# Performance work log

Hardware: AMD Instinct MI355X
Metric: run time of the kernel (lower is better)

## Reference

```python
import jax, jax.numpy as jnp
import numpy as np

NUM_HEADS = 16
HEAD_DIM = 80  # embed_dim 1280 / 16


def setup_inputs() -> dict:
    key = jax.random.key(0)
    ks = jax.random.split(key, 5)
    E = NUM_HEADS * HEAD_DIM
    sq, b = 1024, 8
    x = jax.random.normal(ks[0], (sq, b, E), dtype=jnp.float32)
    w_in = jax.random.normal(ks[1], (E, 3 * E), dtype=jnp.float32) * (E ** -0.5)
    b_in = jax.random.normal(ks[2], (3 * E,), dtype=jnp.float32) * 0.01
    w_out = jax.random.normal(ks[3], (E, E), dtype=jnp.float32) * (E ** -0.5)
    b_out = jax.random.normal(ks[4], (E,), dtype=jnp.float32) * 0.01
    return {"x": x, "w_in": w_in, "b_in": b_in, "w_out": w_out, "b_out": b_out}


def reference(x, w_in, b_in, w_out, b_out):
    sq, b, E = x.shape
    H, D = NUM_HEADS, HEAD_DIM
    norm_factor = jnp.asarray(D ** 0.5, x.dtype)
    # in_proj: [sq, b, 3E] -> [sq, b, H, 3D], split into q/k/v along last dim
    mixed = (x @ w_in + b_in).reshape(sq, b, H, 3 * D)
    q, k, v = jnp.split(mixed, 3, axis=-1)  # each [sq, b, H, D]
    # merge (b, H) and move to batch-of-bmm layout [b*H, sq, D]
    q = q.reshape(sq, b * H, D).transpose(1, 0, 2) / norm_factor
    k = k.reshape(sq, b * H, D).transpose(1, 0, 2)
    v = v.reshape(sq, b * H, D).transpose(1, 0, 2)
    scores = jnp.einsum('nqd,nkd->nqk', q, k)  # [b*H, sq, sq]
    probs = jax.nn.softmax(scores, axis=-1)
    ctx = jnp.einsum('nqk,nkd->nqd', probs, v)  # [b*H, sq, D]
    # [b, H, sq, D] -> [sq, b, H, D] -> [sq, b, E]
    ctx = ctx.reshape(b, H, sq, D).transpose(2, 0, 1, 3).reshape(sq, b, E)
    return ctx @ w_out + b_out
```

## Files before the change

kernel.cpp:

```cpp
#include <hip/hip_runtime.h>

#define DEVI __device__ __forceinline__

typedef _Float16 f16x8 __attribute__((ext_vector_type(8)));
typedef _Float16 f16x4v __attribute__((ext_vector_type(4)));
typedef _Float16 f16x2 __attribute__((ext_vector_type(2)));
typedef __fp16 fp16x2 __attribute__((ext_vector_type(2)));
typedef float f32x4 __attribute__((ext_vector_type(4)));
typedef float f32x16 __attribute__((ext_vector_type(16)));
typedef unsigned u32x4 __attribute__((ext_vector_type(4)));

DEVI void gl16(const void* g, void* l) {
  __builtin_amdgcn_global_load_lds((const __attribute__((address_space(1))) void*)g,
                                   (__attribute__((address_space(3))) void*)l, 16, 0, 0);
}

#define VMCNT(N) asm volatile("s_waitcnt vmcnt(" #N ")" ::: "memory")
#define LGKM0() asm volatile("s_waitcnt lgkmcnt(0)" ::: "memory")
#define BARRIER() asm volatile("s_barrier" ::: "memory")

#if __has_builtin(__builtin_amdgcn_exp2f)
#define EXP2(x) __builtin_amdgcn_exp2f(x)
#else
#define EXP2(x) exp2f(x)
#endif

DEVI unsigned pk2(float a, float b) {
  fp16x2 t = __builtin_amdgcn_cvt_pkrtz(a, b);
  return __builtin_bit_cast(unsigned, t);
}
DEVI void pl32swap(unsigned &a, unsigned &b) {
  asm volatile("v_permlane32_swap_b32 %0, %1" : "+v"(a), "+v"(b));
}
DEVI float max3f(float a, float b, float c) {
  float d;
  asm("v_max3_f32 %0, %1, %2, %3" : "=v"(d) : "v"(a), "v"(b), "v"(c));
  return d;
}

__global__ __launch_bounds__(256) void k_prep(const float* __restrict__ x, _Float16* __restrict__ xb,
                                              const float* __restrict__ w_in, _Float16* __restrict__ w_inT,
                                              const float* __restrict__ w_out, _Float16* __restrict__ w_outT) {
  __shared__ float t[32][33];
  int bid = blockIdx.x;
  int tid = threadIdx.x;
  if (bid < 2048) {
    const int n4 = 8192 * 1280 / 4;
    for (int i = bid * 256 + tid; i < n4; i += 2048 * 256) {
      float4 v = ((const float4*)x)[i];
      f16x4v h = { (_Float16)v.x, (_Float16)v.y, (_Float16)v.z, (_Float16)v.w };
      ((f16x4v*)xb)[i] = h;
    }
    return;
  }
  const float* in; _Float16* out; int R, C, tIdx; bool perm;
  if (bid < 6848) { in = w_in;  out = w_inT;  R = 1280; C = 3840; tIdx = bid - 2048; perm = true; }
  else            { in = w_out; out = w_outT; R = 1280; C = 1280; tIdx = bid - 6848; perm = false; }
  int ntc = C / 32;
  int cb = (tIdx % ntc) * 32, rb = (tIdx / ntc) * 32;
  int tx = tid & 31, ty = tid >> 5;
  #pragma unroll
  for (int i = ty; i < 32; i += 8) t[i][tx] = in[(size_t)(rb + i) * C + cb + tx];
  __syncthreads();
  #pragma unroll
  for (int i = ty; i < 32; i += 8) {
    int c = cb + i;
    if (perm) {
      int hq = c / 240, tt = c - hq * 240;
      int reg = tt / 80, d = tt - reg * 80;
      c = reg * 1280 + hq * 80 + d;
    }
    out[(size_t)c * R + rb + tx] = (_Float16)t[tx][i];
  }
}


#define MM(NLO, AF, BF) do {                                                                       \
    __builtin_amdgcn_s_setprio(1);                                                                 \
    _Pragma("unroll")                                                                              \
    for (int m_ = 0; m_ < 8; m_++) {                                                               \
      acc[m_][NLO]     = __builtin_amdgcn_mfma_f32_16x16x32_f16(AF[m_], BF[NLO],     acc[m_][NLO],     0, 0, 0); \
      acc[m_][NLO + 1] = __builtin_amdgcn_mfma_f32_16x16x32_f16(AF[m_], BF[NLO + 1], acc[m_][NLO + 1], 0, 0, 0); \
    }                                                                                              \
    __builtin_amdgcn_s_setprio(0);                                                                 \
  } while (0)

#define LDA(KT, KK, DST) do {                                                                      \
    const _Float16* bas_ = &smem[(size_t)((((KT) & 1) * 2) + wr) * 8192];                          \
    _Pragma("unroll")                                                                              \
    for (int m_ = 0; m_ < 8; m_++)                                                                 \
      DST[m_] = *(const f16x8*)&bas_[(m_ * 16 + ln) * 64 + (((((KK) * 4) + g) ^ chB) << 3)];       \
  } while (0)

#define LDB(KT, KK, DST) do {                                                                      \
    const _Float16* bas_ = &smem[32768 + (size_t)((((KT) & 1) * 2) + (wc >> 1)) * 8192];           \
    _Pragma("unroll")                                                                              \
    for (int n_ = 0; n_ < 4; n_++)                                                                 \
      DST[n_] = *(const f16x8*)&bas_[((wc & 1) * 64 + n_ * 16 + ln) * 64 + (((((KK) * 4) + g) ^ chB) << 3)]; \
  } while (0)

template<int M, int N, int K>
__global__ __launch_bounds__(512, 2) void k_gemm8(const _Float16* __restrict__ A, const _Float16* __restrict__ BT,
                                                  const float* __restrict__ bias,
                                                  _Float16* __restrict__ qo, _Float16* __restrict__ ko,
                                                  _Float16* __restrict__ vo) {
  extern __shared__ _Float16 smem[];
  constexpr int NT = K / 64;
  constexpr int NI = NT / 2;
  const int tid = threadIdx.x;
  const int w = tid >> 6, lane = tid & 63, ln = lane & 15, g = lane >> 4;
  const int wr = w >> 2, wc = w & 3;
  const int l8 = lane >> 3, l7 = lane & 7;
  const int stChunk = (l7 ^ l8) << 3;
  const int chB = ln & 7;

  constexpr int MT = M / 256;
  const int xcd = blockIdx.x & 7;
  const int i = blockIdx.x >> 3;
  const int bm0 = (xcd * (MT / 8) + (i & 3)) * 256;
  const int bn0 = (i >> 2) * 256;

  auto stgA = [&](int kt, int hh) {
    _Float16* ldsb = &smem[(size_t)((kt & 1) * 2 + hh) * 8192 + w * 1024];
    const _Float16* g0 = &A[(size_t)(bm0 + hh * 128 + w * 16 + l8) * K + kt * 64 + stChunk];
    gl16(g0, ldsb);
    gl16(g0 + (size_t)8 * K, ldsb + 512);
  };
  auto stgB = [&](int kt, int hh) {
    _Float16* ldsb = &smem[32768 + (size_t)((kt & 1) * 2 + hh) * 8192 + w * 1024];
    const _Float16* g0 = &BT[(size_t)(bn0 + hh * 128 + w * 16 + l8) * K + kt * 64 + stChunk];
    gl16(g0, ldsb);
    gl16(g0 + (size_t)8 * K, ldsb + 512);
  };

  f32x4 acc[8][4] = {};
  f16x8 a0[8], a1[8], b0[4], b1[4];

  stgB(0, 0); stgB(0, 1); stgA(0, 0); stgA(0, 1);
  stgB(1, 0); stgB(1, 1); stgA(1, 0);
  VMCNT(6);
  BARRIER();
  LDA(0, 0, a0); LDB(0, 0, b0);

  for (int it = 0; it < NI; ++it) {
    const int T0 = 2 * it, T1 = 2 * it + 1;
    const int S0 = (T0 + 2 < NT) ? T0 + 2 : 0;
    const int S1 = (T1 + 2 < NT) ? T1 + 2 : 1;
    LDB(T0, 1, b1);
    stgA(T1, 1);
    BARRIER();
    MM(0, a0, b0);
    LGKM0(); BARRIER();
    LDA(T0, 1, a1);
    stgB(S0, 0);
    BARRIER();
    MM(2, a0, b0);
    LGKM0(); BARRIER();
    stgB(S0, 1);
    BARRIER();
    MM(0, a1, b1);
    VMCNT(4);
    LGKM0(); BARRIER();
    LDA(T1, 0, a0); LDB(T1, 0, b0);
    stgA(S0, 0);
    BARRIER();
    MM(2, a1, b1);
    LGKM0(); BARRIER();
    LDB(T1, 1, b1);
    stgA(S0, 1);
    BARRIER();
    MM(0, a0, b0);
    LGKM0(); BARRIER();
    LDA(T1, 1, a1);
    stgB(S1, 0);
    BARRIER();
    MM(2, a0, b0);
    LGKM0(); BARRIER();
    stgB(S1, 1);
    BARRIER();
    MM(0, a1, b1);
    VMCNT(4);
    LGKM0(); BARRIER();
    LDA(S0, 0, a0); LDB(S0, 0, b0);
    stgA(S1, 0);
    BARRIER();
    MM(2, a1, b1);
    LGKM0(); BARRIER();
  }

  VMCNT(0);
  BARRIER();
  _Float16* sH = smem;
  const int regn = bn0 / 1280;
  const int relb = bn0 - regn * 1280;
  #pragma unroll
  for (int n = 0; n < 4; n++) {
    int col = wc * 64 + n * 16 + ln;
    int rel = relb + col;
    int h = rel / 80, d = rel - h * 80;
    float bv = bias[h * 240 + regn * 80 + d];
    float scl = (regn == 0) ? (0.11180339887498948f * 1.4426950408889634f) : 1.0f;
    #pragma unroll
    for (int m = 0; m < 8; m++) {
      #pragma unroll
      for (int r = 0; r < 4; r++) {
        int row = wr * 128 + m * 16 + 4 * g + r;
        sH[row * 256 + col] = (_Float16)((acc[m][n][r] + bv) * scl);
      }
    }
  }
  LGKM0();
  BARRIER();
  _Float16* dst = (regn == 0) ? qo : (regn == 1) ? ko : vo;
  #pragma unroll
  for (int i2 = 0; i2 < 16; i2++) {
    int id = tid + 512 * i2;
    int row = id >> 5, c8 = id & 31;
    f16x8 v = *(const f16x8*)&sH[row * 256 + c8 * 8];
    int rel = relb + c8 * 8;
    int h = rel / 80, d0 = rel - h * 80;
    int grow = bm0 + row;
    *(f16x8*)&dst[(size_t)(((grow & 7) * 16 + h) * 1024 + (grow >> 3)) * 80 + d0] = v;
  }
}


#define MMo(NLO, AF, BF) do {                                                                      \
    __builtin_amdgcn_s_setprio(1);                                                                 \
    _Pragma("unroll")                                                                              \
    for (int m_ = 0; m_ < 4; m_++) {                                                               \
      acc[m_][NLO]     = __builtin_amdgcn_mfma_f32_16x16x32_f16(AF[m_], BF[NLO],     acc[m_][NLO],     0, 0, 0); \
      acc[m_][NLO + 1] = __builtin_amdgcn_mfma_f32_16x16x32_f16(AF[m_], BF[NLO + 1], acc[m_][NLO + 1], 0, 0, 0); \
    }                                                                                              \
    __builtin_amdgcn_s_setprio(0);                                                                 \
  } while (0)

#define LDAo(KT, KK, DST) do {                                                                     \
    const _Float16* bas_ = &smem[(size_t)((KT) & 1) * 8192];                                       \
    _Pragma("unroll")                                                                              \
    for (int m_ = 0; m_ < 4; m_++)                                                                 \
      DST[m_] = *(const f16x8*)&bas_[(wr * 64 + m_ * 16 + ln) * 64 + (((((KK) * 4) + g) ^ chB) << 3)]; \
  } while (0)

#define LDBo(KT, KK, DST) do {                                                                     \
    const _Float16* bas_ = &smem[16384 + (size_t)(((KT) & 1) * 2 + (wc >> 1)) * 8192];             \
    _Pragma("unroll")                                                                              \
    for (int n_ = 0; n_ < 4; n_++)                                                                 \
      DST[n_] = *(const f16x8*)&bas_[((wc & 1) * 64 + n_ * 16 + ln) * 64 + (((((KK) * 4) + g) ^ chB) << 3)]; \
  } while (0)

template<int M, int N, int K>
__global__ __launch_bounds__(512, 2) void k_gemm8o(const _Float16* __restrict__ A, const _Float16* __restrict__ BT,
                                                   const float* __restrict__ bias, float* __restrict__ outF) {
  extern __shared__ _Float16 smem[];
  constexpr int NT = K / 64;
  constexpr int NI = NT / 2;
  const int tid = threadIdx.x;
  const int w = tid >> 6, lane = tid & 63, ln = lane & 15, g = lane >> 4;
  const int wr = w >> 2, wc = w & 3;
  const int l8 = lane >> 3, l7 = lane & 7;
  const int stChunk = (l7 ^ l8) << 3;
  const int chB = ln & 7;

  const int xcd = blockIdx.x & 7;
  const int i = blockIdx.x >> 3;
  const int bm0 = (xcd * 8 + (i & 7)) * 128;
  const int bn0 = (i >> 3) * 256;

  auto stgA = [&](int kt) {
    _Float16* ldsb = &smem[(size_t)(kt & 1) * 8192 + w * 1024];
    const _Float16* g0 = &A[(size_t)(bm0 + w * 16 + l8) * K + kt * 64 + stChunk];
    gl16(g0, ldsb);
    gl16(g0 + (size_t)8 * K, ldsb + 512);
  };
  auto stgB = [&](int kt, int hh) {
    _Float16* ldsb = &smem[16384 + (size_t)((kt & 1) * 2 + hh) * 8192 + w * 1024];
    const _Float16* g0 = &BT[(size_t)(bn0 + hh * 128 + w * 16 + l8) * K + kt * 64 + stChunk];
    gl16(g0, ldsb);
    gl16(g0 + (size_t)8 * K, ldsb + 512);
  };

  f32x4 acc[4][4] = {};
  f16x8 a0[4], a1[4], b0[4], b1[4];

  stgB(0, 0); stgB(0, 1); stgA(0);
  stgB(1, 0); stgB(1, 1); stgA(1);
  VMCNT(6);
  BARRIER();
  LDAo(0, 0, a0); LDBo(0, 0, b0);

  for (int it = 0; it < NI; ++it) {
    const int T0 = 2 * it, T1 = 2 * it + 1;
    const int S0 = (T0 + 2 < NT) ? T0 + 2 : 0;
    const int S1 = (T1 + 2 < NT) ? T1 + 2 : 1;
    LDBo(T0, 1, b1);
    BARRIER(); MMo(0, a0, b0); LGKM0(); BARRIER();
    LDAo(T0, 1, a1);
    stgB(S0, 0);
    BARRIER(); MMo(2, a0, b0); LGKM0(); BARRIER();
    stgB(S0, 1);
    BARRIER(); MMo(0, a1, b1); VMCNT(4); LGKM0(); BARRIER();
    LDAo(T1, 0, a0); LDBo(T1, 0, b0);
    stgA(S0);
    BARRIER(); MMo(2, a1, b1); LGKM0(); BARRIER();
    LDBo(T1, 1, b1);
    BARRIER(); MMo(0, a0, b0); LGKM0(); BARRIER();
    LDAo(T1, 1, a1);
    stgB(S1, 0);
    BARRIER(); MMo(2, a0, b0); LGKM0(); BARRIER();
    stgB(S1, 1);
    BARRIER(); MMo(0, a1, b1); VMCNT(4); LGKM0(); BARRIER();
    LDAo(S0, 0, a0); LDBo(S0, 0, b0);
    stgA(S1);
    BARRIER(); MMo(2, a1, b1); LGKM0(); BARRIER();
  }

  VMCNT(0);
  #pragma unroll
  for (int n = 0; n < 4; n++) {
    int col = bn0 + wc * 64 + n * 16 + ln;
    float bv = bias[col];
    #pragma unroll
    for (int m = 0; m < 4; m++) {
      int rbase = bm0 + wr * 64 + m * 16 + 4 * g;
      #pragma unroll
      for (int r = 0; r < 4; r++)
        outF[(size_t)(rbase + r) * N + col] = acc[m][n][r] + bv;
    }
  }
}

__global__ __launch_bounds__(512, 2) void k_attn(const _Float16* __restrict__ qb, const _Float16* __restrict__ kb,
                                                 const _Float16* __restrict__ vb, _Float16* __restrict__ ctxg) {
  extern __shared__ _Float16 smem[];
  _Float16* Kb0 = smem;
  _Float16* Kb1 = smem + 8192;
  _Float16* Vb0 = smem + 16384;
  _Float16* Vb1 = smem + 16384 + 6144;

  const int tid = threadIdx.x;
  const int w = tid >> 6, lane = tid & 63;
  const int l32 = lane & 31, h = lane >> 5;
  const int lx = l32 & 7;
  const int xcd = blockIdx.x & 7;
  const int j = blockIdx.x >> 3;
  const int head = xcd + 8 * (j & 15);
  const int s0 = (j >> 4) * 256;
  const int bb = head >> 4, h16 = head & 15;
  const size_t hbase = (size_t)head * 81920;

  const int cA = tid;
  const int cB = (tid < 128) ? tid + 512 : tid;
  const int sA = cA & 63, dA = cA >> 6;
  const int sB = cB & 63, dB = cB >> 6;
  const _Float16* kGA = kb + hbase + sA * 80 + dA * 8;
  const _Float16* kGB = kb + hbase + sB * 80 + dB * 8;
  const int kOA = sA * 128 + ((dA ^ (sA & 7)) << 3);
  const int kOB = sB * 128 + ((dB ^ (sB & 7)) << 3);

  const int s4 = tid & 15, dc = tid >> 4;
  const _Float16* vG = vb + hbase + (s4 * 4) * 80 + dc * 8;

  uint4 krA, krB, vq0, vq1, vq2, vq3;
  auto issue = [&](int kt) {
    krA = *(const uint4*)(kGA + kt * 5120);
    krB = *(const uint4*)(kGB + kt * 5120);
    if (tid < 160) {
      const _Float16* p = vG + kt * 5120;
      vq0 = *(const uint4*)(p);
      vq1 = *(const uint4*)(p + 80);
      vq2 = *(const uint4*)(p + 160);
      vq3 = *(const uint4*)(p + 240);
    }
  };
  auto stage = [&](int b) {
    _Float16* kd = b ? Kb1 : Kb0;
    _Float16* vd = b ? Vb1 : Vb0;
    *(uint4*)(kd + kOA) = krA;
    *(uint4*)(kd + kOB) = krB;
    if (tid < 160) {
      const unsigned* w0 = (const unsigned*)&vq0;
      const unsigned* w1 = (const unsigned*)&vq1;
      const unsigned* w2 = (const unsigned*)&vq2;
      const unsigned* w3 = (const unsigned*)&vq3;
      #pragma unroll
      for (int jj = 0; jj < 8; ++jj) {
        int jw = jj >> 1;
        unsigned lo, hi;
        if (jj & 1) {
          lo = (w0[jw] >> 16) | (w1[jw] & 0xffff0000u);
          hi = (w2[jw] >> 16) | (w3[jw] & 0xffff0000u);
        } else {
          lo = (w0[jw] & 0xffffu) | (w1[jw] << 16);
          hi = (w2[jw] & 0xffffu) | (w3[jw] << 16);
        }
        unsigned long long u = (unsigned long long)lo | ((unsigned long long)hi << 32);
        int d = dc * 8 + jj;
        *(unsigned long long*)(vd + d * 64 + (((s4 >> 1) ^ jj) << 3) + ((s4 & 1) << 2)) = u;
      }
    }
  };

  const int qrow = s0 + w * 32 + l32;
  f16x8 qf[5];
  #pragma unroll
  for (int s = 0; s < 5; s++)
    qf[s] = *(const f16x8*)&qb[(size_t)(head * 1024 + qrow) * 80 + s * 16 + h * 8];

  f32x16 ct[3] = {};
  float m_run = -INFINITY;

  issue(0);
  stage(0);
  if (tid < 64) {
    Vb0[80 * 64 + tid] = (_Float16)1.0f;
    Vb1[80 * 64 + tid] = (_Float16)1.0f;
  }
  LGKM0();
  BARRIER();
  issue(1);

  for (int kt = 0; kt < 16; ++kt) {
    const _Float16* kc = (kt & 1) ? Kb1 : Kb0;
    const _Float16* vc = (kt & 1) ? Vb1 : Vb0;

    f32x16 sc0 = {}, sc1 = {};
    __builtin_amdgcn_s_setprio(1);
    #pragma unroll
    for (int s = 0; s < 5; ++s) {
      f16x8 kf0 = *(const f16x8*)&kc[l32 * 128 + (((2 * s + h) ^ lx) << 3)];
      f16x8 kf1 = *(const f16x8*)&kc[(32 + l32) * 128 + (((2 * s + h) ^ lx) << 3)];
      sc0 = __builtin_amdgcn_mfma_f32_32x32x16_f16(kf0, qf[s], sc0, 0, 0, 0);
      sc1 = __builtin_amdgcn_mfma_f32_32x32x16_f16(kf1, qf[s], sc1, 0, 0, 0);
    }
    __builtin_amdgcn_s_setprio(0);

    if (kt < 15) stage((kt + 1) & 1);
    if (kt < 14) issue(kt + 2);

    float t0 = max3f(sc0[0], sc0[1], sc0[2]);
    float t1 = max3f(sc0[3], sc0[4], sc0[5]);
    float t2 = max3f(sc0[6], sc0[7], sc0[8]);
    float t3 = max3f(sc0[9], sc0[10], sc0[11]);
    float t4 = max3f(sc0[12], sc0[13], sc0[14]);
    float t5 = max3f(sc0[15], sc1[0], sc1[1]);
    float t6 = max3f(sc1[2], sc1[3], sc1[4]);
    float t7 = max3f(sc1[5], sc1[6], sc1[7]);
    float t8 = max3f(sc1[8], sc1[9], sc1[10]);
    float t9 = max3f(sc1[11], sc1[12], sc1[13]);
    float ta = fmaxf(sc1[14], sc1[15]);
    float u0 = max3f(t0, t1, t2);
    float u1 = max3f(t3, t4, t5);
    float u2 = max3f(t6, t7, t8);
    float tm = fmaxf(max3f(u0, u1, u2), fmaxf(t9, ta));
    tm = fmaxf(tm, __shfl_xor(tm, 32));

    if (__any(tm > m_run + 8.f)) {
      float mnew = fmaxf(m_run, tm);
      float fac = EXP2(m_run - mnew);
      #pragma unroll
      for (int dt = 0; dt < 3; ++dt)
        #pragma unroll
        for (int i = 0; i < 16; ++i) ct[dt][i] *= fac;
      m_run = mnew;
    }

    float p0[16], p1[16];
    #pragma unroll
    for (int i = 0; i < 16; ++i) p0[i] = EXP2(sc0[i] - m_run);
    #pragma unroll
    for (int i = 0; i < 16; ++i) p1[i] = EXP2(sc1[i] - m_run);

    unsigned fr[4][4];
    #define PACK4(T, PP) do {                                                \
        _Pragma("unroll")                                                    \
        for (int s16 = 0; s16 < 2; ++s16) {                                  \
          unsigned u0_ = pk2(PP[8 * s16 + 0], PP[8 * s16 + 1]);              \
          unsigned u1_ = pk2(PP[8 * s16 + 2], PP[8 * s16 + 3]);              \
          unsigned u2_ = pk2(PP[8 * s16 + 4], PP[8 * s16 + 5]);              \
          unsigned u3_ = pk2(PP[8 * s16 + 6], PP[8 * s16 + 7]);              \
          pl32swap(u0_, u2_); pl32swap(u1_, u3_);                            \
          fr[2 * (T) + s16][0] = u0_; fr[2 * (T) + s16][1] = u1_;            \
          fr[2 * (T) + s16][2] = u2_; fr[2 * (T) + s16][3] = u3_;            \
        }                                                                    \
      } while (0)
    PACK4(0, p0);
    PACK4(1, p1);

    __builtin_amdgcn_s_setprio(1);
    #pragma unroll
    for (int ss = 0; ss < 4; ++ss) {
      u32x4 fu = { fr[ss][0], fr[ss][1], fr[ss][2], fr[ss][3] };
      f16x8 pf = __builtin_bit_cast(f16x8, fu);
      #pragma unroll
      for (int dt = 0; dt < 3; ++dt) {
        f16x8 vf = *(const f16x8*)&vc[(dt * 32 + l32) * 64 + (((2 * ss + h) ^ lx) << 3)];
        ct[dt] = __builtin_amdgcn_mfma_f32_32x32x16_f16(vf, pf, ct[dt], 0, 0, 0);
      }
    }
    __builtin_amdgcn_s_setprio(0);

    if (kt < 15) {
      LGKM0();
      BARRIER();
    }
  }

  float lsum = __shfl(ct[2][8], l32);
  float inv = 1.f / lsum;
  int sq = s0 + w * 32 + l32;
  _Float16* outp = ctxg + (size_t)(sq * 8 + bb) * 1280 + h16 * 80 + 4 * h;
  #pragma unroll
  for (int dt = 0; dt < 3; ++dt)
    #pragma unroll
    for (int rq = 0; rq < 4; ++rq) {
      if (dt == 2 && rq >= 2) continue;
      f16x4v o = { (_Float16)(ct[dt][rq * 4 + 0] * inv), (_Float16)(ct[dt][rq * 4 + 1] * inv),
                   (_Float16)(ct[dt][rq * 4 + 2] * inv), (_Float16)(ct[dt][rq * 4 + 3] * inv) };
      *(f16x4v*)&outp[dt * 32 + rq * 8] = o;
    }
}

extern "C" void kernel_launch(void* const* d_in, const int* in_sizes, int n_in,
                              void* d_out, int out_size, void* d_ws, size_t ws_size,
                              hipStream_t stream) {
  const float* x     = (const float*)d_in[0];
  const float* w_in  = (const float*)d_in[1];
  const float* b_in  = (const float*)d_in[2];
  const float* w_out = (const float*)d_in[3];
  const float* b_out = (const float*)d_in[4];
  float* out = (float*)d_out;

  char* ws = (char*)d_ws;
  size_t off = 0;
  auto carve = [&](size_t bytes) -> void* {
    void* p = ws + off;
    off += (bytes + 255) & ~(size_t)255;
    return p;
  };
  _Float16* xb     = (_Float16*)carve(8192ull * 1280 * 2);
  _Float16* w_inT  = (_Float16*)carve(3840ull * 1280 * 2);
  _Float16* w_outT = (_Float16*)carve(1280ull * 1280 * 2);
  _Float16* qb     = (_Float16*)carve(128ull * 1024 * 80 * 2);
  _Float16* kbuf   = (_Float16*)carve(128ull * 1024 * 80 * 2);
  _Float16* vbuf   = (_Float16*)carve(128ull * 1024 * 80 * 2);
  _Float16* ctxg   = (_Float16*)carve(8192ull * 1280 * 2);
  if (off > ws_size) return;

  hipFuncSetAttribute(reinterpret_cast<const void*>(&k_gemm8<8192, 3840, 1280>),
                      hipFuncAttributeMaxDynamicSharedMemorySize, 131072);
  hipFuncSetAttribute(reinterpret_cast<const void*>(&k_gemm8o<8192, 1280, 1280>),
                      hipFuncAttributeMaxDynamicSharedMemorySize, 98304);
  hipFuncSetAttribute(reinterpret_cast<const void*>(&k_attn),
                      hipFuncAttributeMaxDynamicSharedMemorySize, 57344);

  k_prep<<<8448, 256, 0, stream>>>(x, xb, w_in, w_inT, w_out, w_outT);

  k_gemm8<8192, 3840, 1280><<<480, 512, 131072, stream>>>(xb, w_inT, b_in, qb, kbuf, vbuf);
  k_attn<<<512, 512, 57344, stream>>>(qb, kbuf, vbuf, ctxg);
  k_gemm8o<8192, 1280, 1280><<<320, 512, 98304, stream>>>(ctxg, w_outT, b_out, out);
}
```

Measured before the change: 229.0 us.

## Restructure GEMM main loops to batch global-to-LDS stages per k-tile

Both projection GEMM kernels get a new software pipeline. Instead of interleaving one global-to-LDS stage between each quarter of MFMA work, each k-tile's A and B loads are issued together after a full tile's MFMAs. The change uses fewer barriers, pairs the MM calls, and sets the wait counts to match. It aims to cut barrier and wait overhead, but it batches memory traffic into bursts and may overlap global loads less well with compute.

Measured after the change: 235.9 us. 1.03x slower.

```diff
diff --git a/kernel.cpp b/kernel.cpp
--- a/kernel.cpp
+++ b/kernel.cpp
@@ -136,9 +136,9 @@
   f32x4 acc[8][4] = {};
   f16x8 a0[8], a1[8], b0[4], b1[4];
 
-  stgB(0, 0); stgB(0, 1); stgA(0, 0); stgA(0, 1);
-  stgB(1, 0); stgB(1, 1); stgA(1, 0);
-  VMCNT(6);
+  stgA(0, 0); stgA(0, 1); stgB(0, 0); stgB(0, 1);
+  stgA(1, 0); stgA(1, 1); stgB(1, 0); stgB(1, 1);
+  VMCNT(8);
   BARRIER();
   LDA(0, 0, a0); LDB(0, 0, b0);
 
@@ -146,45 +146,25 @@
     const int T0 = 2 * it, T1 = 2 * it + 1;
     const int S0 = (T0 + 2 < NT) ? T0 + 2 : 0;
     const int S1 = (T1 + 2 < NT) ? T1 + 2 : 1;
-    LDB(T0, 1, b1);
-    stgA(T1, 1);
-    BARRIER();
-    MM(0, a0, b0);
-    LGKM0(); BARRIER();
-    LDA(T0, 1, a1);
-    stgB(S0, 0);
-    BARRIER();
-    MM(2, a0, b0);
-    LGKM0(); BARRIER();
-    stgB(S0, 1);
-    BARRIER();
-    MM(0, a1, b1);
-    VMCNT(4);
-    LGKM0(); BARRIER();
+    LDB(T0, 1, b1); LDA(T0, 1, a1);
+    BARRIER();
+    MM(0, a0, b0); MM(2, a0, b0);
+    LGKM0(); BARRIER();
+    stgA(S0, 0); stgA(S0, 1); stgB(S0, 0); stgB(S0, 1);
+    VMCNT(8);
+    BARRIER();
     LDA(T1, 0, a0); LDB(T1, 0, b0);
-    stgA(S0, 0);
-    BARRIER();
-    MM(2, a1, b1);
-    LGKM0(); BARRIER();
-    LDB(T1, 1, b1);
-    stgA(S0, 1);
-    BARRIER();
-    MM(0, a0, b0);
-    LGKM0(); BARRIER();
-    LDA(T1, 1, a1);
-    stgB(S1, 0);
-    BARRIER();
-    MM(2, a0, b0);
-    LGKM0(); BARRIER();
-    stgB(S1, 1);
-    BARRIER();
-    MM(0, a1, b1);
-    VMCNT(4);
-    LGKM0(); BARRIER();
+    MM(0, a1, b1); MM(2, a1, b1);
+    LGKM0(); BARRIER();
+    LDB(T1, 1, b1); LDA(T1, 1, a1);
+    BARRIER();
+    MM(0, a0, b0); MM(2, a0, b0);
+    LGKM0(); BARRIER();
+    stgA(S1, 0); stgA(S1, 1); stgB(S1, 0); stgB(S1, 1);
+    VMCNT(8);
+    BARRIER();
     LDA(S0, 0, a0); LDB(S0, 0, b0);
-    stgA(S1, 0);
-    BARRIER();
-    MM(2, a1, b1);
+    MM(0, a1, b1); MM(2, a1, b1);
     LGKM0(); BARRIER();
   }
 
@@ -283,8 +263,8 @@
   f32x4 acc[4][4] = {};
   f16x8 a0[4], a1[4], b0[4], b1[4];
 
-  stgB(0, 0); stgB(0, 1); stgA(0);
-  stgB(1, 0); stgB(1, 1); stgA(1);
+  stgA(0); stgB(0, 0); stgB(0, 1);
+  stgA(1); stgB(1, 0); stgB(1, 1);
   VMCNT(6);
   BARRIER();
   LDAo(0, 0, a0); LDBo(0, 0, b0);
@@ -293,26 +273,26 @@
     const int T0 = 2 * it, T1 = 2 * it + 1;
     const int S0 = (T0 + 2 < NT) ? T0 + 2 : 0;
     const int S1 = (T1 + 2 < NT) ? T1 + 2 : 1;
-    LDBo(T0, 1, b1);
-    BARRIER(); MMo(0, a0, b0); LGKM0(); BARRIER();
-    LDAo(T0, 1, a1);
-    stgB(S0, 0);
-    BARRIER(); MMo(2, a0, b0); LGKM0(); BARRIER();
-    stgB(S0, 1);
-    BARRIER(); MMo(0, a1, b1); VMCNT(4); LGKM0(); BARRIER();
+    LDBo(T0, 1, b1); LDAo(T0, 1, a1);
+    BARRIER();
+    MMo(0, a0, b0); MMo(2, a0, b0);
+    LGKM0(); BARRIER();
+    stgA(S0); stgB(S0, 0); stgB(S0, 1);
+    VMCNT(6);
+    BARRIER();
     LDAo(T1, 0, a0); LDBo(T1, 0, b0);
-    stgA(S0);
-    BARRIER(); MMo(2, a1, b1); LGKM0(); BARRIER();
-    LDBo(T1, 1, b1);
-    BARRIER(); MMo(0, a0, b0); LGKM0(); BARRIER();
-    LDAo(T1, 1, a1);
-    stgB(S1, 0);
-    BARRIER(); MMo(2, a0, b0); LGKM0(); BARRIER();
-    stgB(S1, 1);
-    BARRIER(); MMo(0, a1, b1); VMCNT(4); LGKM0(); BARRIER();
+    MMo(0, a1, b1); MMo(2, a1, b1);
+    LGKM0(); BARRIER();
+    LDBo(T1, 1, b1); LDAo(T1, 1, a1);
+    BARRIER();
+    MMo(0, a0, b0); MMo(2, a0, b0);
+    LGKM0(); BARRIER();
+    stgA(S1); stgB(S1, 0); stgB(S1, 1);
+    VMCNT(6);
+    BARRIER();
     LDAo(S0, 0, a0); LDBo(S0, 0, b0);
-    stgA(S1);
-    BARRIER(); MMo(2, a1, b1); LGKM0(); BARRIER();
+    MMo(0, a1, b1); MMo(2, a1, b1);
+    LGKM0(); BARRIER();
   }
 
   VMCNT(0);
```
